# Performance work log

Hardware: AMD Instinct MI355X
Metric: run time of the kernel (lower is better)

Reference implementation:

```python
import jax, jax.numpy as jnp
import numpy as np


def setup_inputs() -> dict:
    key = jax.random.key(0)
    k1, k2 = jax.random.split(key)
    B, T, D, K = 16, 4096, 1024, 512
    h = jax.random.normal(k1, (B, T, D), dtype=jnp.float32)
    codebook = jax.random.normal(k2, (K, D), dtype=jnp.float32)
    return {"h": h, "codebook": codebook}


def reference(h, codebook):
    """SAMMCodebook.encode: nearest-codeword indices via squared L2 distance.

    h: [B, T, D]; codebook: [K, D] -> z: [B, T] int32
    """
    B, T, D = h.shape
    h_flat = h.reshape(-1, D)                                  # [N, D]
    h_sq = jnp.sum(h_flat * h_flat, axis=-1, keepdims=True)    # [N, 1]
    c_sq = jnp.sum(codebook * codebook, axis=-1)[None, :]      # [1, K]
    # dist[n,k] = ||h_n||^2 + ||c_k||^2 - 2 <h_n, c_k>
    dist = h_sq + c_sq - 2.0 * (h_flat @ codebook.T)           # [N, K]
    z = jnp.argmin(dist, axis=-1).reshape(B, T)
    return z.astype(jnp.int32)
```

## Files before the change

### kernel.cpp

```cpp
#include <hip/hip_runtime.h>


#define D_DIM 1024
#define K_CB  512
#define DELTA 4.0f
#define MAXC_IN 15
#define FULLSCAN 0xFFFFu

typedef __attribute__((ext_vector_type(8))) short short8;
typedef __attribute__((ext_vector_type(4))) float floatx4;

#define WS_CBB  0ull
#define WS_CSQ  1048576ull

typedef const unsigned int __attribute__((address_space(1)))* gaddr_t;
typedef unsigned int __attribute__((address_space(3)))* laddr_t;
static __device__ __forceinline__ void async_copy16(const void* g, void* l) {
    __builtin_amdgcn_global_load_lds((gaddr_t)g, (laddr_t)l, 16, 0, 0);
}

static __device__ __forceinline__ unsigned f2bf(float f) {
    unsigned u = __builtin_bit_cast(unsigned, f);
    return (u + 0x7FFFu + ((u >> 16) & 1u)) >> 16;
}

__global__ __launch_bounds__(256)
void prep_kernel(const float* __restrict__ cb, unsigned short* __restrict__ cbb,
                 float* __restrict__ csq) {
    __shared__ float red[4];
    const int k = blockIdx.x, t = threadIdx.x;
    const float4 v = *(const float4*)(cb + (size_t)k * D_DIM + t * 4);
    uint2 u;
    u.x = f2bf(v.x) | (f2bf(v.y) << 16);
    u.y = f2bf(v.z) | (f2bf(v.w) << 16);
    *(uint2*)(cbb + (size_t)k * D_DIM + t * 4) = u;
    float s = v.x * v.x + v.y * v.y + v.z * v.z + v.w * v.w;
    #pragma unroll
    for (int off = 32; off > 0; off >>= 1) s += __shfl_down(s, off, 64);
    if ((t & 63) == 0) red[t >> 6] = s;
    __syncthreads();
    if (t == 0) csq[k] = red[0] + red[1] + red[2] + red[3];
}

__global__ __launch_bounds__(256, 2)
void coarse_kernel(const float* __restrict__ h,
                   const unsigned short* __restrict__ cbb,
                   const float* __restrict__ csq,
                   const float* __restrict__ cb,
                   int* __restrict__ out) {
    __shared__ unsigned char smem[81920] __attribute__((aligned(16)));
    unsigned short* As = (unsigned short*)smem;
    unsigned short* Bs = (unsigned short*)(smem + 16384);

    const int tid = threadIdx.x;
    const int w = tid >> 6, lane = tid & 63;
    const int l15 = lane & 15, kq = lane >> 4;
    const size_t row0 = (size_t)blockIdx.x * 64;
    const int wc_ = w * 128;

    const int qp8 = (kq ^ ((l15 >> 1) & 3)) * 8;

    const int qsrc = (lane & 3) ^ ((lane >> 3) & 3);
    const int brow = w * 128 + (lane >> 2);
    const unsigned char* cbb_b = (const unsigned char*)cbb;
    const size_t bsrc_base = ((size_t)brow * D_DIM + qsrc * 8) * 2;

    const int ar = tid >> 2, aq4 = (tid & 3) * 4;
    const float* gA = h + (row0 + ar) * D_DIM + (tid & 3) * 32;
    const int aswz = l15 & 7;

    floatx4 acc[4][8];
    #pragma unroll
    for (int i = 0; i < 4; ++i)
        #pragma unroll
        for (int j = 0; j < 8; ++j) acc[i][j] = (floatx4){0.f, 0.f, 0.f, 0.f};

#define ISSUE_B(dkn, par) \
    _Pragma("unroll") \
    for (int j = 0; j < 8; ++j) \
        async_copy16(cbb_b + bsrc_base + (size_t)j * (16 * D_DIM * 2) + (size_t)(dkn) * 2, \
                     Bs + (par) * 16384 + (w * 128 + j * 16) * 32);

#define STAGE_A(cc) do { \
    floatx4 av[8]; \
    _Pragma("unroll") \
    for (int k = 0; k < 8; ++k) \
        av[k] = __builtin_nontemporal_load((const floatx4*)(gA + (cc) * 128 + k * 4)); \
    _Pragma("unroll") \
    for (int j = 0; j < 4; ++j) { \
        uint4 u; \
        u.x = f2bf(av[2 * j].x)     | (f2bf(av[2 * j].y) << 16); \
        u.y = f2bf(av[2 * j].z)     | (f2bf(av[2 * j].w) << 16); \
        u.z = f2bf(av[2 * j + 1].x) | (f2bf(av[2 * j + 1].y) << 16); \
        u.w = f2bf(av[2 * j + 1].z) | (f2bf(av[2 * j + 1].w) << 16); \
        const int ps = (aq4 + j) ^ (ar & 7); \
        *(uint4*)(As + ar * 128 + ps * 8) = u; \
    } \
} while (0)

#define INNER_STEP(ii, PF) do { \
    if (PF) { \
        ISSUE_B((c4 + (ii) + 1) * 32, ((ii) + 1) & 1); \
        asm volatile("s_waitcnt vmcnt(8)" ::: "memory"); \
    } else { \
        asm volatile("s_waitcnt vmcnt(0)" ::: "memory"); \
    } \
    __builtin_amdgcn_sched_barrier(0); \
    short8 a[4], b[8]; \
    _Pragma("unroll") \
    for (int rt = 0; rt < 4; ++rt) \
        a[rt] = *(const short8*)(As + (rt * 16 + l15) * 128 + ((((ii) * 4 + kq)) ^ aswz) * 8); \
    _Pragma("unroll") \
    for (int ct = 0; ct < 8; ++ct) \
        b[ct] = *(const short8*)(Bs + ((ii) & 1) * 16384 + (wc_ + ct * 16 + l15) * 32 + qp8); \
    __builtin_amdgcn_s_setprio(1); \
    _Pragma("unroll") \
    for (int rt = 0; rt < 4; ++rt) \
        _Pragma("unroll") \
        for (int ct = 0; ct < 8; ++ct) \
            acc[rt][ct] = __builtin_amdgcn_mfma_f32_16x16x32_bf16( \
                a[rt], b[ct], acc[rt][ct], 0, 0, 0); \
    __builtin_amdgcn_s_setprio(0); \
} while (0)

    ISSUE_B(0, 0);

    for (int c = 0; c < 7; ++c) {
        const int c4 = c * 4;
        STAGE_A(c);
        __syncthreads();
        INNER_STEP(0, true);
        INNER_STEP(1, true);
        INNER_STEP(2, true);
        INNER_STEP(3, true);
        __syncthreads();
    }
    {
        const int c4 = 28;
        STAGE_A(7);
        __syncthreads();
        INNER_STEP(0, true);
        INNER_STEP(1, true);
        INNER_STEP(2, true);
        INNER_STEP(3, false);
    }

#undef INNER_STEP
#undef STAGE_A
#undef ISSUE_B

    float k1[16], k2[16];
    unsigned cpk[16];
    #pragma unroll
    for (int i = 0; i < 16; ++i) { k1[i] = 3.4e38f; k2[i] = 3.4e38f; cpk[i] = 0; }
    #pragma unroll
    for (int ct = 0; ct < 8; ++ct) {
        const int col = wc_ + ct * 16 + l15;
        const float cq = csq[col];
        #pragma unroll
        for (int rt = 0; rt < 4; ++rt)
            #pragma unroll
            for (int reg = 0; reg < 4; ++reg) {
                const float s = fmaf(-2.0f, acc[rt][ct][reg], cq);
                const int ri = rt * 4 + reg;
                if (s < k1[ri]) {
                    k2[ri] = k1[ri]; k1[ri] = s;
                    cpk[ri] = (cpk[ri] << 16) | (unsigned)col;
                } else if (s < k2[ri]) {
                    k2[ri] = s;
                    cpk[ri] = (cpk[ri] & 0xFFFFu) | ((unsigned)col << 16);
                }
            }
    }

    float* mval = (float*)smem;
    int*   mcol = (int*)(smem + 33024);
    unsigned short* ccnt  = (unsigned short*)(smem + 66048);
    unsigned short* clist = (unsigned short*)(smem + 66176);
    __syncthreads();
    #pragma unroll
    for (int rt = 0; rt < 4; ++rt)
        #pragma unroll
        for (int reg = 0; reg < 4; ++reg) {
            const int ri = rt * 4 + reg;
            const int r = rt * 16 + kq * 4 + reg;
            const int e = (w * 16 + l15) * 2;
            mval[r * 129 + e] = k1[ri];
            mcol[r * 129 + e] = (int)(cpk[ri] & 0xFFFFu);
            mval[r * 129 + e + 1] = k2[ri];
            mcol[r * 129 + e + 1] = (int)(cpk[ri] >> 16);
        }
    __syncthreads();

    if (tid < 64) {
        const int r = tid;
        float bv = mval[r * 129]; int bc = mcol[r * 129];
        for (int e = 1; e < 128; ++e) {
            const float v = mval[r * 129 + e];
            const int   c = mcol[r * 129 + e];
            if (v < bv || (v == bv && c < bc)) { bv = v; bc = c; }
        }
        const float thr = bv + DELTA;
        int others = 0;
        for (int e = 0; e < 128; ++e) {
            const float v = mval[r * 129 + e];
            const int   c = mcol[r * 129 + e];
            if (v < thr && c != bc) {
                if (others < MAXC_IN) clist[r * 16 + 1 + others] = (unsigned short)c;
                ++others;
            }
        }
        if (others == 0) {
            out[row0 + r] = bc;
            ccnt[r] = 0;
        } else if (others <= MAXC_IN) {
            clist[r * 16] = (unsigned short)bc;
            ccnt[r] = (unsigned short)(others + 1);
        } else {
            ccnt[r] = (unsigned short)FULLSCAN;
        }
    }
    __syncthreads();

    for (int r = w; r < 64; r += 4) {
        const unsigned cnt = ccnt[r];
        if (cnt == 0) continue;
        const size_t grow = row0 + r;
        const float* hrow = h + grow * D_DIM;
        float4 hv[4];
        #pragma unroll
        for (int j = 0; j < 4; ++j)
            hv[j] = *(const float4*)(hrow + j * 256 + lane * 4);
        float bs = 3.4e38f; int bc = 0x7fffffff;
        const bool full = (cnt == FULLSCAN);
        const int total = full ? K_CB : (int)cnt;
        for (int i = 0; i < total; ++i) {
            const int c = full ? i : (int)clist[r * 16 + i];
            const float* crow = cb + (size_t)c * D_DIM;
            float d = 0.0f;
            #pragma unroll
            for (int j = 0; j < 4; ++j) {
                const float4 cv = *(const float4*)(crow + j * 256 + lane * 4);
                d = fmaf(hv[j].x, cv.x, d);
                d = fmaf(hv[j].y, cv.y, d);
                d = fmaf(hv[j].z, cv.z, d);
                d = fmaf(hv[j].w, cv.w, d);
            }
            #pragma unroll
            for (int off = 32; off > 0; off >>= 1) d += __shfl_down(d, off, 64);
            d = __shfl(d, 0, 64);
            const float sc = fmaf(-2.0f, d, csq[c]);
            if (sc < bs || (sc == bs && c < bc)) { bs = sc; bc = c; }
        }
        if (lane == 0) out[grow] = bc;
    }
}

extern "C" void kernel_launch(void* const* d_in, const int* in_sizes, int n_in,
                              void* d_out, int out_size, void* d_ws, size_t ws_size,
                              hipStream_t stream) {
    const float* h  = (const float*)d_in[0];
    const float* cb = (const float*)d_in[1];
    int* out = (int*)d_out;
    unsigned char* ws = (unsigned char*)d_ws;
    const int nrows = in_sizes[0] / D_DIM;

    unsigned short* cbb = (unsigned short*)(ws + WS_CBB);
    float* csq = (float*)(ws + WS_CSQ);

    prep_kernel<<<dim3(K_CB), dim3(256), 0, stream>>>(cb, cbb, csq);
    coarse_kernel<<<dim3(nrows / 64), dim3(256), 0, stream>>>(
        h, cbb, csq, cb, out);
}
```

Baseline: 512.7 us.

## Software-pipeline A tile staging per 32-wide k-step with double-buffered LDS

Replaces the chunked A staging (load 128 columns of h, convert to bf16, barrier, then four MFMA steps) with a per-32-column pipeline. Each step prefetches the next A slice into registers alongside the async B copy, runs its MFMAs, then converts and publishes the next A slice into a second LDS buffer before a single barrier. The goal is to hide global-load latency of h behind the MFMA work and remove the bulk staging stall, and it also shrinks the LDS footprint. The cost is a barrier on every k-step instead of twice per four steps, plus finer-grained vmcnt bookkeeping that has to stay correct.

```diff
diff --git a/kernel.cpp b/kernel.cpp
--- a/kernel.cpp
+++ b/kernel.cpp
@@ -48,9 +48,9 @@
                    const float* __restrict__ csq,
                    const float* __restrict__ cb,
                    int* __restrict__ out) {
-    __shared__ unsigned char smem[81920] __attribute__((aligned(16)));
+    __shared__ unsigned char smem[73728] __attribute__((aligned(16)));
     unsigned short* As = (unsigned short*)smem;
-    unsigned short* Bs = (unsigned short*)(smem + 16384);
+    unsigned short* Bs = (unsigned short*)(smem + 8192);
 
     const int tid = threadIdx.x;
     const int w = tid >> 6, lane = tid & 63;
@@ -60,20 +60,22 @@
 
     const int qp8 = (kq ^ ((l15 >> 1) & 3)) * 8;
 
+    const int ar = tid >> 2, aql = tid & 3;
+    const float* gA = h + (row0 + ar) * D_DIM + aql * 8;
+    const int awoff = ar * 32 + (aql ^ ((ar >> 1) & 3)) * 8;
+
     const int qsrc = (lane & 3) ^ ((lane >> 3) & 3);
     const int brow = w * 128 + (lane >> 2);
     const unsigned char* cbb_b = (const unsigned char*)cbb;
     const size_t bsrc_base = ((size_t)brow * D_DIM + qsrc * 8) * 2;
 
-    const int ar = tid >> 2, aq4 = (tid & 3) * 4;
-    const float* gA = h + (row0 + ar) * D_DIM + (tid & 3) * 32;
-    const int aswz = l15 & 7;
-
     floatx4 acc[4][8];
     #pragma unroll
     for (int i = 0; i < 4; ++i)
         #pragma unroll
         for (int j = 0; j < 8; ++j) acc[i][j] = (floatx4){0.f, 0.f, 0.f, 0.f};
+
+    float4 va0, va1;
 
 #define ISSUE_B(dkn, par) \
     _Pragma("unroll") \
@@ -81,27 +83,34 @@
         async_copy16(cbb_b + bsrc_base + (size_t)j * (16 * D_DIM * 2) + (size_t)(dkn) * 2, \
                      Bs + (par) * 16384 + (w * 128 + j * 16) * 32);
 
-#define STAGE_A(cc) do { \
-    floatx4 av[8]; \
-    _Pragma("unroll") \
-    for (int k = 0; k < 8; ++k) \
-        av[k] = __builtin_nontemporal_load((const floatx4*)(gA + (cc) * 128 + k * 4)); \
-    _Pragma("unroll") \
-    for (int j = 0; j < 4; ++j) { \
-        uint4 u; \
-        u.x = f2bf(av[2 * j].x)     | (f2bf(av[2 * j].y) << 16); \
-        u.y = f2bf(av[2 * j].z)     | (f2bf(av[2 * j].w) << 16); \
-        u.z = f2bf(av[2 * j + 1].x) | (f2bf(av[2 * j + 1].y) << 16); \
-        u.w = f2bf(av[2 * j + 1].z) | (f2bf(av[2 * j + 1].w) << 16); \
-        const int ps = (aq4 + j) ^ (ar & 7); \
-        *(uint4*)(As + ar * 128 + ps * 8) = u; \
-    } \
+#define LOAD_A(dkn) do { \
+    va0 = *(const float4*)(gA + (dkn)); \
+    va1 = *(const float4*)(gA + (dkn) + 4); \
 } while (0)
 
-#define INNER_STEP(ii, PF) do { \
-    if (PF) { \
-        ISSUE_B((c4 + (ii) + 1) * 32, ((ii) + 1) & 1); \
-        asm volatile("s_waitcnt vmcnt(8)" ::: "memory"); \
+#define PUB_A(par) do { \
+    uint4 u; \
+    u.x = f2bf(va0.x) | (f2bf(va0.y) << 16); \
+    u.y = f2bf(va0.z) | (f2bf(va0.w) << 16); \
+    u.z = f2bf(va1.x) | (f2bf(va1.y) << 16); \
+    u.w = f2bf(va1.z) | (f2bf(va1.w) << 16); \
+    *(uint4*)(As + (par) * 2048 + awoff) = u; \
+} while (0)
+
+    LOAD_A(0);
+    ISSUE_B(0, 0);
+    asm volatile("s_waitcnt vmcnt(8)" ::: "memory");
+    __builtin_amdgcn_sched_barrier(0);
+    PUB_A(0);
+    asm volatile("s_waitcnt lgkmcnt(0)" ::: "memory");
+    __builtin_amdgcn_s_barrier();
+    __builtin_amdgcn_sched_barrier(0);
+
+#define STEP(p, s, LAST) do { \
+    if (!(LAST)) { \
+        LOAD_A(((s) + 1) * 32); \
+        ISSUE_B(((s) + 1) * 32, (p) ^ 1); \
+        asm volatile("s_waitcnt vmcnt(10)" ::: "memory");   \
     } else { \
         asm volatile("s_waitcnt vmcnt(0)" ::: "memory"); \
     } \
@@ -109,10 +118,10 @@
     short8 a[4], b[8]; \
     _Pragma("unroll") \
     for (int rt = 0; rt < 4; ++rt) \
-        a[rt] = *(const short8*)(As + (rt * 16 + l15) * 128 + ((((ii) * 4 + kq)) ^ aswz) * 8); \
+        a[rt] = *(const short8*)(As + (p) * 2048 + (rt * 16 + l15) * 32 + qp8); \
     _Pragma("unroll") \
     for (int ct = 0; ct < 8; ++ct) \
-        b[ct] = *(const short8*)(Bs + ((ii) & 1) * 16384 + (wc_ + ct * 16 + l15) * 32 + qp8); \
+        b[ct] = *(const short8*)(Bs + (p) * 16384 + (wc_ + ct * 16 + l15) * 32 + qp8); \
     __builtin_amdgcn_s_setprio(1); \
     _Pragma("unroll") \
     for (int rt = 0; rt < 4; ++rt) \
@@ -121,32 +130,26 @@
             acc[rt][ct] = __builtin_amdgcn_mfma_f32_16x16x32_bf16( \
                 a[rt], b[ct], acc[rt][ct], 0, 0, 0); \
     __builtin_amdgcn_s_setprio(0); \
+    if (!(LAST)) { \
+        asm volatile("s_waitcnt vmcnt(8)" ::: "memory");    \
+        __builtin_amdgcn_sched_barrier(0); \
+        PUB_A((p) ^ 1); \
+    } \
+    asm volatile("s_waitcnt lgkmcnt(0)" ::: "memory");      \
+    __builtin_amdgcn_s_barrier(); \
+    __builtin_amdgcn_sched_barrier(0); \
 } while (0)
 
-    ISSUE_B(0, 0);
-
-    for (int c = 0; c < 7; ++c) {
-        const int c4 = c * 4;
-        STAGE_A(c);
-        __syncthreads();
-        INNER_STEP(0, true);
-        INNER_STEP(1, true);
-        INNER_STEP(2, true);
-        INNER_STEP(3, true);
-        __syncthreads();
-    }
-    {
-        const int c4 = 28;
-        STAGE_A(7);
-        __syncthreads();
-        INNER_STEP(0, true);
-        INNER_STEP(1, true);
-        INNER_STEP(2, true);
-        INNER_STEP(3, false);
-    }
-
-#undef INNER_STEP
-#undef STAGE_A
+    for (int s2 = 0; s2 < 15; ++s2) {
+        STEP(0, 2 * s2, false);
+        STEP(1, 2 * s2 + 1, false);
+    }
+    STEP(0, 30, false);
+    STEP(1, 31, true);
+
+#undef STEP
+#undef PUB_A
+#undef LOAD_A
 #undef ISSUE_B
 
     float k1[16], k2[16];
```

Measured after the change: 463.0 us. 9.7% less time.
